# Optimization experiments

Measured on AMD Instinct MI355X. Metric: run time of the kernel, lower is better.

## Reference

```python
import jax, jax.numpy as jnp
import numpy as np

EPS = 1e-5
NEG = -1e20


def layer_norm(x, gamma, beta):
    mu = jnp.mean(x, axis=-1, keepdims=True)
    var = jnp.mean(jnp.square(x - mu), axis=-1, keepdims=True)
    return (x - mu) * jax.lax.rsqrt(var + EPS) * gamma + beta


def setup_inputs() -> dict:
    key = jax.random.key(0)
    ks = jax.random.split(key, 12)
    B, S, D, H, HD = 2, 2048, 1024, 16, 64
    hid = H * HD
    inp = {
        "q": jax.random.normal(ks[0], (B, S, D), jnp.float32),
        "k": jax.random.normal(ks[1], (B, S, D), jnp.float32),
        "v": jax.random.normal(ks[2], (B, S, D), jnp.float32),
        "mask": jax.random.randint(ks[3], (B, 1, S, S), 0, 2, jnp.int32),
        "Wq": jax.random.normal(ks[4], (D, hid), jnp.float32) * (D ** -0.5),
        "bq": jnp.zeros((hid,), jnp.float32),
        "Wk": jax.random.normal(ks[5], (D, hid), jnp.float32) * (D ** -0.5),
        "bk": jnp.zeros((hid,), jnp.float32),
        "Wv": jax.random.normal(ks[6], (D, hid), jnp.float32) * (D ** -0.5),
        "bv": jnp.zeros((hid,), jnp.float32),
        "Wo": jax.random.normal(ks[7], (hid, D), jnp.float32) * (hid ** -0.5),
        "bo": jnp.zeros((D,), jnp.float32),
        "gamma": jnp.ones((D,), jnp.float32),
        "beta": jnp.zeros((D,), jnp.float32),
    }
    return inp


def reference(q, k, v, mask, Wq, bq, Wk, bk, Wv, bv, Wo, bo, gamma, beta):
    B, S, D = q.shape
    H, HD = 16, 64
    scale = HD ** -0.5
    qh = (layer_norm(q, gamma, beta) @ Wq + bq).reshape(B, S, H, HD).transpose(0, 2, 1, 3)
    kh = (layer_norm(k, gamma, beta) @ Wk + bk).reshape(B, S, H, HD).transpose(0, 2, 1, 3)
    vh = (layer_norm(v, gamma, beta) @ Wv + bv).reshape(B, S, H, HD).transpose(0, 2, 1, 3)
    dots = jnp.einsum('bhqd,bhkd->bhqk', qh, kh)  # [B,H,S,S]
    dots = jnp.where(mask == 0, NEG, dots) * scale  # mask BEFORE scale (as in source)
    attn = jax.nn.softmax(dots, axis=-1)
    out = jnp.einsum('bhqk,bhkd->bhqd', attn, vh)  # [B,H,S,HD]
    # Faithful to `out.view(B, S, -1)` on a [B,H,S,HD]-contiguous tensor: raw reshape,
    # no head transpose.
    out = out.reshape(B, S, H * HD)
    return out @ Wo + bo
```

## Files before the change

### kernel.cpp

```cpp
#include <hip/hip_runtime.h>

typedef short short8 __attribute__((ext_vector_type(8)));
typedef float f32x4 __attribute__((ext_vector_type(4)));

#define QSCALE 0.18033688011112042f

__device__ __forceinline__ unsigned short f2bf(float f) {
  unsigned u = __builtin_bit_cast(unsigned, f);
  u += 0x7fffu + ((u >> 16) & 1u);
  return (unsigned short)(u >> 16);
}

__device__ __forceinline__ void gload16(const void* g, void* l) {
  typedef __attribute__((address_space(1))) unsigned int gas;
  typedef __attribute__((address_space(3))) unsigned int las;
  __builtin_amdgcn_global_load_lds((gas*)(unsigned long long)g,
                                   (las*)(unsigned)(unsigned long long)l, 16, 0, 0);
}

__device__ __forceinline__ short8 mk8(unsigned r0, unsigned r1, unsigned r2, unsigned r3) {
  union { unsigned u[4]; short8 s; } t;
  t.u[0] = r0; t.u[1] = r1; t.u[2] = r2; t.u[3] = r3;
  return t.s;
}

#define MFMA16(a, b, c) __builtin_amdgcn_mfma_f32_16x16x32_bf16(a, b, c, 0, 0, 0)

__global__ __launch_bounds__(256) void wtrans_kernel(
    const float* __restrict__ Wq, const float* __restrict__ Wk,
    const float* __restrict__ Wv, const float* __restrict__ Wo,
    unsigned short* __restrict__ Wt) {
  const int wsel = blockIdx.z;
  const float* W = wsel == 0 ? Wq : wsel == 1 ? Wk : wsel == 2 ? Wv : Wo;
  const float wscale = (wsel == 0) ? QSCALE : 1.0f;
  unsigned short* out = Wt + (long)wsel * 1048576;
  __shared__ float lds[64][65];
  const int t = threadIdx.x;
  const int k0 = blockIdx.x * 64, n0 = blockIdx.y * 64;
#pragma unroll
  for (int i = 0; i < 4; ++i) {
    int r = (t >> 4) + i * 16, c4 = (t & 15) * 4;
    float4 vv = *(const float4*)(W + (long)(k0 + r) * 1024 + n0 + c4);
    lds[r][c4] = vv.x; lds[r][c4 + 1] = vv.y; lds[r][c4 + 2] = vv.z; lds[r][c4 + 3] = vv.w;
  }
  __syncthreads();
#pragma unroll
  for (int i = 0; i < 16; ++i) {
    int flat = t + i * 256;
    int n = flat >> 6, kk = flat & 63;
    out[(long)(n0 + n) * 1024 + k0 + kk] = f2bf(lds[kk][n] * wscale);
  }
}

__global__ __launch_bounds__(256) void maskpack_kernel(const int* __restrict__ mask,
                                                       unsigned* __restrict__ bits) {
  const long n = 8388608;
  const long stride = (long)gridDim.x * 256;
  const int lane = threadIdx.x & 63;
  for (long i = (long)blockIdx.x * 256 + threadIdx.x; i < n; i += stride) {
    unsigned long long bal = __ballot(mask[i] != 0);
    if ((lane & 31) == 0) bits[i >> 5] = (unsigned)(bal >> (lane & 32));
  }
}

__global__ __launch_bounds__(256) void ln_kernel(
    const float* __restrict__ q, const float* __restrict__ k, const float* __restrict__ v,
    const float* __restrict__ gamma, const float* __restrict__ beta,
    unsigned short* __restrict__ lnq, unsigned short* __restrict__ lnk,
    unsigned short* __restrict__ lnv) {
  const int row = blockIdx.x, which = blockIdx.y;
  const float* x = (which == 0 ? q : which == 1 ? k : v) + (long)row * 1024;
  unsigned short* y = (which == 0 ? lnq : which == 1 ? lnk : lnv) + (long)row * 1024;
  const int t = threadIdx.x, lane = t & 63, wv = t >> 6;
  float4 xv = ((const float4*)x)[t];
  float s = xv.x + xv.y + xv.z + xv.w;
  float s2 = xv.x * xv.x + xv.y * xv.y + xv.z * xv.z + xv.w * xv.w;
#pragma unroll
  for (int off = 32; off > 0; off >>= 1) {
    s += __shfl_down(s, off);
    s2 += __shfl_down(s2, off);
  }
  __shared__ float red[8];
  if (lane == 0) { red[wv] = s; red[wv + 4] = s2; }
  __syncthreads();
  float tot = red[0] + red[1] + red[2] + red[3];
  float tot2 = red[4] + red[5] + red[6] + red[7];
  float mu = tot * (1.0f / 1024.0f);
  float var = tot2 * (1.0f / 1024.0f) - mu * mu;
  float rs = rsqrtf(var + 1e-5f);
  float4 g = ((const float4*)gamma)[t];
  float4 be = ((const float4*)beta)[t];
  ushort4 o;
  o.x = f2bf((xv.x - mu) * rs * g.x + be.x);
  o.y = f2bf((xv.y - mu) * rs * g.y + be.y);
  o.z = f2bf((xv.z - mu) * rs * g.z + be.z);
  o.w = f2bf((xv.w - mu) * rs * g.w + be.w);
  ((ushort4*)y)[t] = o;
}

template <int BM, int MODE>
__global__ __launch_bounds__(256) void gemm_kernel(
    const unsigned short* __restrict__ A0, const unsigned short* __restrict__ A1,
    const unsigned short* __restrict__ A2, const unsigned short* __restrict__ Wt,
    const float* __restrict__ b0, const float* __restrict__ b1,
    const float* __restrict__ b2, unsigned short* __restrict__ outB,
    unsigned short* __restrict__ outV, float* __restrict__ outF) {
  constexpr int MI = BM / 32;
  constexpr int NT = 32;
  constexpr int ACHA = BM / 64;
  const int z = blockIdx.z;
  const unsigned short* A = z == 0 ? A0 : z == 1 ? A1 : A2;
  const unsigned short* Bt = Wt + (long)z * 1048576;
  const float* bias = z == 0 ? b0 : z == 1 ? b1 : b2;
  unsigned short* outz = outB + (long)z * 4194304;
  const float bscale = (MODE == 0 && z == 0) ? QSCALE : 1.0f;

  __shared__ char lds[(BM + 128) * 128];
  char* As = lds;
  char* Bs = lds + BM * 128;
  const int tid = threadIdx.x, lane = tid & 63, w = tid >> 6;
  const int g = lane >> 4;
  const int wr = w >> 1, wc = w & 1;
  const int m0 = blockIdx.x * BM, n0 = blockIdx.y * 128;

  f32x4 acc[MI][4] = {};

#define GSTAGE(KT, BUF)                                                       \
  {                                                                           \
    _Pragma("unroll") for (int i = 0; i < ACHA; ++i) {                        \
      int cc = tid + i * 256;                                                 \
      int row = cc >> 2, p = cc & 3;                                          \
      int kk = p ^ ((row >> 1) & 3);                                          \
      gload16(A + (long)(m0 + row) * 1024 + (KT)*32 + kk * 8,                 \
              As + (BUF) * (BM * 64) + cc * 16);                              \
    }                                                                         \
    _Pragma("unroll") for (int i = 0; i < 2; ++i) {                           \
      int cc = tid + i * 256;                                                 \
      int row = cc >> 2, p = cc & 3;                                          \
      int kk = p ^ ((row >> 1) & 3);                                          \
      gload16(Bt + (long)(n0 + row) * 1024 + (KT)*32 + kk * 8,                \
              Bs + (BUF)*8192 + cc * 16);                                     \
    }                                                                         \
  }

  GSTAGE(0, 0);
  asm volatile("s_waitcnt vmcnt(0)" ::: "memory");
  __builtin_amdgcn_s_barrier();

  for (int kt = 0; kt < NT; ++kt) {
    const int cur = kt & 1;
    if (kt + 1 < NT) GSTAGE(kt + 1, cur ^ 1);
    short8 af[MI], bf[4];
#pragma unroll
    for (int mi = 0; mi < MI; ++mi) {
      int row = wr * (BM / 2) + mi * 16 + (lane & 15);
      int part = g ^ ((row >> 1) & 3);
      af[mi] = *(const short8*)(As + cur * (BM * 64) + row * 64 + part * 16);
    }
#pragma unroll
    for (int ni = 0; ni < 4; ++ni) {
      int row = wc * 64 + ni * 16 + (lane & 15);
      int part = g ^ ((row >> 1) & 3);
      bf[ni] = *(const short8*)(Bs + cur * 8192 + row * 64 + part * 16);
    }
    __builtin_amdgcn_s_setprio(1);
#pragma unroll
    for (int mi = 0; mi < MI; ++mi)
#pragma unroll
      for (int ni = 0; ni < 4; ++ni)
        acc[mi][ni] = MFMA16(af[mi], bf[ni], acc[mi][ni]);
    __builtin_amdgcn_s_setprio(0);
    asm volatile("s_waitcnt vmcnt(0) lgkmcnt(0)" ::: "memory");
    __builtin_amdgcn_s_barrier();
  }
#undef GSTAGE

#pragma unroll
  for (int mi = 0; mi < MI; ++mi) {
    int mbase = m0 + wr * (BM / 2) + mi * 16 + ((lane >> 4) << 2);
#pragma unroll
    for (int ni = 0; ni < 4; ++ni) {
      int j = n0 + wc * 64 + ni * 16 + (lane & 15);
      float bj = bias[j] * bscale;
      float t0 = acc[mi][ni][0] + bj;
      float t1 = acc[mi][ni][1] + bj;
      float t2 = acc[mi][ni][2] + bj;
      float t3 = acc[mi][ni][3] + bj;
      if constexpr (MODE == 0) {
        int b = mbase >> 11, s = mbase & 2047;
        int h = j >> 6, d = j & 63;
        if (z == 2) {
          unsigned lo, hi;
          asm("v_cvt_pk_bf16_f32 %0, %1, %2" : "=v"(lo) : "v"(t0), "v"(t1));
          asm("v_cvt_pk_bf16_f32 %0, %1, %2" : "=v"(hi) : "v"(t2), "v"(t3));
          uint2 o; o.x = lo; o.y = hi;
          int sp = (s & ~31) | (((s >> 2) & 3) << 3) | (((s >> 4) & 1) << 2);
          *(uint2*)(outV + ((long)(b * 16 + h) * 64 + d) * 2048 + sp) = o;
        } else {
          long base = (((long)(b * 16 + h)) * 2048 + s) * 64 + d;
          outz[base] = f2bf(t0);
          outz[base + 64] = f2bf(t1);
          outz[base + 128] = f2bf(t2);
          outz[base + 192] = f2bf(t3);
        }
      } else {
        outF[(long)mbase * 1024 + j] = t0;
        outF[(long)(mbase + 1) * 1024 + j] = t1;
        outF[(long)(mbase + 2) * 1024 + j] = t2;
        outF[(long)(mbase + 3) * 1024 + j] = t3;
      }
    }
  }
}

__global__ __launch_bounds__(256, 2) void attn_kernel(
    const unsigned short* __restrict__ qh, const unsigned short* __restrict__ kh,
    const unsigned short* __restrict__ vt, const unsigned* __restrict__ mbits,
    unsigned short* __restrict__ O) {
  constexpr int S = 2048, NT = 32;
  __shared__ char lds[32768];
  char* Ks = lds;
  char* Vts = lds + 16384;
  const int tid = threadIdx.x, lane = tid & 63, w = tid >> 6;
  const int g = lane >> 4, c = lane & 15;

  const int flat = blockIdx.y * 16 + blockIdx.x;
  const int fl2 = (flat & 7) * 64 + (flat >> 3);
  const int qb = fl2 & 15, bh = fl2 >> 4, b = bh >> 4;
  const int kt0 = (fl2 & 3) * 8;

  const unsigned short* qp = qh + (long)bh * S * 64;
  const unsigned short* kp = kh + (long)bh * S * 64;
  const unsigned short* vp = vt + (long)bh * 64 * S;
  unsigned short* op = O + (long)bh * S * 64;
  const unsigned* mrow = mbits + (long)b * S * 64;
  const int q0 = qb * 128 + w * 32;
  const int myq0 = q0 + c, myq1 = q0 + 16 + c;

  short8 bq_[2][2];
#pragma unroll
  for (int qg = 0; qg < 2; ++qg)
#pragma unroll
    for (int ds = 0; ds < 2; ++ds)
      bq_[qg][ds] = *(const short8*)(qp + (long)(q0 + qg * 16 + c) * 64 + ds * 32 + g * 8);

  f32x4 o_acc[2][4] = {};
  float lp0 = 0.f, lp1 = 0.f;

#define STAGE(KT, BUF)                                                              \
  {                                                                                 \
    _Pragma("unroll") for (int i = 0; i < 2; ++i) {                                 \
      int cc = tid + i * 256;                                                       \
      int row = cc >> 3, pg = (cc & 7) ^ (row & 7);                                 \
      gload16(kp + (long)((KT)*64 + row) * 64 + pg * 8, Ks + (BUF)*8192 + cc * 16); \
    }                                                                               \
    _Pragma("unroll") for (int i = 0; i < 2; ++i) {                                 \
      int cc = tid + i * 256;                                                       \
      int row = cc >> 3, pg = (cc & 7) ^ (row & 7);                                 \
      gload16(vp + (long)row * S + (KT)*64 + pg * 8, Vts + (BUF)*8192 + cc * 16);   \
    }                                                                               \
  }

#define SOFTMAX(SC, MC, LP, PA0, PA1)                                               \
  {                                                                                 \
    unsigned ws0 = MC.x >> (g * 4), ws1 = MC.y >> (g * 4);                          \
    unsigned pw[8];                                                                 \
    _Pragma("unroll") for (int kf = 0; kf < 4; ++kf) {                              \
      unsigned wsh = ((kf >= 2) ? ws1 : ws0) >> ((kf & 1) * 16);                    \
      float pv0 = __builtin_amdgcn_exp2f(SC[kf][0]);                                \
      float pv1 = __builtin_amdgcn_exp2f(SC[kf][1]);                                \
      float pv2 = __builtin_amdgcn_exp2f(SC[kf][2]);                                \
      float pv3 = __builtin_amdgcn_exp2f(SC[kf][3]);                                \
      pv0 = (wsh & 1u) ? pv0 : 0.f;                                                 \
      pv1 = (wsh & 2u) ? pv1 : 0.f;                                                 \
      pv2 = (wsh & 4u) ? pv2 : 0.f;                                                 \
      pv3 = (wsh & 8u) ? pv3 : 0.f;                                                 \
      LP += (pv0 + pv1) + (pv2 + pv3);                                              \
      asm("v_cvt_pk_bf16_f32 %0, %1, %2" : "=v"(pw[kf * 2]) : "v"(pv0), "v"(pv1));  \
      asm("v_cvt_pk_bf16_f32 %0, %1, %2" : "=v"(pw[kf * 2 + 1]) : "v"(pv2), "v"(pv3)); \
    }                                                                               \
    PA0 = mk8(pw[0], pw[1], pw[2], pw[3]);                                          \
    PA1 = mk8(pw[4], pw[5], pw[6], pw[7]);                                          \
  }

  STAGE(kt0, 0);
  uint2 m0c = *(const uint2*)(mrow + (long)myq0 * 64 + kt0 * 2);
  uint2 m1c = *(const uint2*)(mrow + (long)myq1 * 64 + kt0 * 2);
  uint2 m0n, m1n;

  for (int kt = 0; kt < NT; ++kt) {
    const int cur = kt & 1;
    if (kt + 1 < NT) {
      const int nx = (kt0 + kt + 1) & 31;
      STAGE(nx, cur ^ 1);
      m0n = *(const uint2*)(mrow + (long)myq0 * 64 + nx * 2);
      m1n = *(const uint2*)(mrow + (long)myq1 * 64 + nx * 2);
      asm volatile("s_waitcnt vmcnt(6)" ::: "memory");
    } else {
      asm volatile("s_waitcnt vmcnt(0)" ::: "memory");
    }
    __builtin_amdgcn_s_barrier();

    f32x4 sc0[4] = {}, sc1[4] = {};
    const char* Kb = Ks + cur * 8192;
    __builtin_amdgcn_s_setprio(1);
#pragma unroll
    for (int ds = 0; ds < 2; ++ds) {
#pragma unroll
      for (int kf = 0; kf < 4; ++kf) {
        int row = kf * 16 + c;
        int part = (ds * 4 + g) ^ (row & 7);
        short8 ak = *(const short8*)(Kb + row * 128 + part * 16);
        sc0[kf] = MFMA16(ak, bq_[0][ds], sc0[kf]);
        sc1[kf] = MFMA16(ak, bq_[1][ds], sc1[kf]);
      }
    }
    __builtin_amdgcn_s_setprio(0);

    short8 pa00, pa01, pa10, pa11;
    SOFTMAX(sc0, m0c, lp0, pa00, pa01);
    SOFTMAX(sc1, m1c, lp1, pa10, pa11);
    m0c = m0n;
    m1c = m1n;

    const char* Vb = Vts + cur * 8192;
    __builtin_amdgcn_s_setprio(1);
#pragma unroll
    for (int ks = 0; ks < 2; ++ks) {
      short8 paA = ks ? pa01 : pa00;
      short8 paB = ks ? pa11 : pa10;
      int part = ks * 4 + g;
#pragma unroll
      for (int nd = 0; nd < 4; ++nd) {
        int d = nd * 16 + c;
        short8 bv = *(const short8*)(Vb + d * 128 + ((part ^ (d & 7)) * 16));
        o_acc[0][nd] = MFMA16(paA, bv, o_acc[0][nd]);
        o_acc[1][nd] = MFMA16(paB, bv, o_acc[1][nd]);
      }
    }
    __builtin_amdgcn_s_setprio(0);

    asm volatile("s_waitcnt lgkmcnt(0)" ::: "memory");
    __builtin_amdgcn_sched_barrier(0);
    __builtin_amdgcn_s_barrier();
  }
#undef SOFTMAX
#undef STAGE

  lp0 += __shfl_xor(lp0, 16);
  lp0 += __shfl_xor(lp0, 32);
  lp1 += __shfl_xor(lp1, 16);
  lp1 += __shfl_xor(lp1, 32);
#pragma unroll
  for (int r = 0; r < 4; ++r) {
    float lr0 = __shfl(lp0, g * 4 + r);
    float lr1 = __shfl(lp1, g * 4 + r);
    float inv0 = 1.0f / lr0;
    float inv1 = 1.0f / lr1;
    int qrow0 = q0 + g * 4 + r;
    int qrow1 = q0 + 16 + g * 4 + r;
#pragma unroll
    for (int nd = 0; nd < 4; ++nd) {
      op[(long)qrow0 * 64 + nd * 16 + c] = f2bf(o_acc[0][nd][r] * inv0);
      op[(long)qrow1 * 64 + nd * 16 + c] = f2bf(o_acc[1][nd][r] * inv1);
    }
  }
}

extern "C" void kernel_launch(void* const* d_in, const int* in_sizes, int n_in,
                              void* d_out, int out_size, void* d_ws, size_t ws_size,
                              hipStream_t stream) {
  const float* q = (const float*)d_in[0];
  const float* k = (const float*)d_in[1];
  const float* v = (const float*)d_in[2];
  const int* mask = (const int*)d_in[3];
  const float* Wq = (const float*)d_in[4];
  const float* bq = (const float*)d_in[5];
  const float* Wk = (const float*)d_in[6];
  const float* bk = (const float*)d_in[7];
  const float* Wv = (const float*)d_in[8];
  const float* bv = (const float*)d_in[9];
  const float* Wo = (const float*)d_in[10];
  const float* bo = (const float*)d_in[11];
  const float* gamma = (const float*)d_in[12];
  const float* beta = (const float*)d_in[13];
  float* out = (float*)d_out;

  char* ws = (char*)d_ws;
  unsigned short* Wt = (unsigned short*)ws;
  unsigned* mbits = (unsigned*)(ws + 8u * 1024 * 1024);
  unsigned short* lnq = (unsigned short*)(ws + 9u * 1024 * 1024);
  unsigned short* lnk = lnq + 4194304;
  unsigned short* lnv = lnk + 4194304;
  unsigned short* qh = lnv + 4194304;
  unsigned short* kh = qh + 4194304;
  unsigned short* vtb = kh + 4194304;
  unsigned short* Ob = lnq;

  wtrans_kernel<<<dim3(16, 16, 4), 256, 0, stream>>>(Wq, Wk, Wv, Wo, Wt);
  maskpack_kernel<<<1024, 256, 0, stream>>>(mask, mbits);
  ln_kernel<<<dim3(4096, 3), 256, 0, stream>>>(q, k, v, gamma, beta, lnq, lnk, lnv);
  gemm_kernel<128, 0><<<dim3(32, 8, 3), 256, 0, stream>>>(lnq, lnk, lnv, Wt, bq, bk, bv,
                                                          qh, vtb, nullptr);
  attn_kernel<<<dim3(16, 32), 256, 0, stream>>>(qh, kh, vtb, mbits, Ob);
  gemm_kernel<64, 1><<<dim3(64, 8, 1), 256, 0, stream>>>(Ob, Ob, Ob, Wt + 3 * 1048576,
                                                         bo, bo, bo, nullptr, nullptr, out);
}
```

Baseline: 139.1 us.

## Triple-buffer GEMM LDS stages to prefetch two k-tiles ahead

```diff
diff --git a/kernel.cpp b/kernel.cpp
--- a/kernel.cpp
+++ b/kernel.cpp
@@ -108,6 +108,7 @@
   constexpr int MI = BM / 32;
   constexpr int NT = 32;
   constexpr int ACHA = BM / 64;
+  constexpr int ABUF = BM * 64;
   const int z = blockIdx.z;
   const unsigned short* A = z == 0 ? A0 : z == 1 ? A1 : A2;
   const unsigned short* Bt = Wt + (long)z * 1048576;
@@ -115,9 +116,9 @@
   unsigned short* outz = outB + (long)z * 4194304;
   const float bscale = (MODE == 0 && z == 0) ? QSCALE : 1.0f;
 
-  __shared__ char lds[(BM + 128) * 128];
+  __shared__ char lds[3 * (BM * 64) + 24576];
   char* As = lds;
-  char* Bs = lds + BM * 128;
+  char* Bs = lds + 3 * ABUF;
   const int tid = threadIdx.x, lane = tid & 63, w = tid >> 6;
   const int g = lane >> 4;
   const int wr = w >> 1, wc = w & 1;
@@ -132,7 +133,7 @@
       int row = cc >> 2, p = cc & 3;                                          \
       int kk = p ^ ((row >> 1) & 3);                                          \
       gload16(A + (long)(m0 + row) * 1024 + (KT)*32 + kk * 8,                 \
-              As + (BUF) * (BM * 64) + cc * 16);                              \
+              As + (BUF)*ABUF + cc * 16);                                     \
     }                                                                         \
     _Pragma("unroll") for (int i = 0; i < 2; ++i) {                           \
       int cc = tid + i * 256;                                                 \
@@ -143,19 +144,30 @@
     }                                                                         \
   }
 
+#define WAIT_STAGE                                                            \
+  if constexpr (BM == 128) {                                                  \
+    asm volatile("s_waitcnt vmcnt(4)" ::: "memory");                          \
+  } else {                                                                    \
+    asm volatile("s_waitcnt vmcnt(3)" ::: "memory");                          \
+  }
+
   GSTAGE(0, 0);
-  asm volatile("s_waitcnt vmcnt(0)" ::: "memory");
+  GSTAGE(1, 1);
+  WAIT_STAGE;
   __builtin_amdgcn_s_barrier();
 
+  int cur = 0;
   for (int kt = 0; kt < NT; ++kt) {
-    const int cur = kt & 1;
-    if (kt + 1 < NT) GSTAGE(kt + 1, cur ^ 1);
+    int sb = cur + 2;
+    if (sb >= 3) sb -= 3;
+    if (kt + 2 < NT) GSTAGE(kt + 2, sb);
+
     short8 af[MI], bf[4];
 #pragma unroll
     for (int mi = 0; mi < MI; ++mi) {
       int row = wr * (BM / 2) + mi * 16 + (lane & 15);
       int part = g ^ ((row >> 1) & 3);
-      af[mi] = *(const short8*)(As + cur * (BM * 64) + row * 64 + part * 16);
+      af[mi] = *(const short8*)(As + cur * ABUF + row * 64 + part * 16);
     }
 #pragma unroll
     for (int ni = 0; ni < 4; ++ni) {
@@ -170,9 +182,17 @@
       for (int ni = 0; ni < 4; ++ni)
         acc[mi][ni] = MFMA16(af[mi], bf[ni], acc[mi][ni]);
     __builtin_amdgcn_s_setprio(0);
-    asm volatile("s_waitcnt vmcnt(0) lgkmcnt(0)" ::: "memory");
+
+    asm volatile("s_waitcnt lgkmcnt(0)" ::: "memory");
+    if (kt + 2 < NT) {
+      WAIT_STAGE;
+    } else if (kt + 1 < NT) {
+      asm volatile("s_waitcnt vmcnt(0)" ::: "memory");
+    }
     __builtin_amdgcn_s_barrier();
-  }
+    cur = (cur + 1 == 3) ? 0 : cur + 1;
+  }
+#undef WAIT_STAGE
 #undef GSTAGE
 
 #pragma unroll
```

Measured after the change: 139.6 us, median of 3. No clear change (+0.4%).
